# Kernel optimization log

Hardware: AMD Instinct MI355X
Metric: run time of the kernel (lower is better)

The kernel has to match this reference:

```python
import jax, jax.numpy as jnp
import numpy as np

B, T, D, S, H = 1024, 365, 5, 27, 256


def setup_inputs() -> dict:
    key = jax.random.key(0)
    ks = jax.random.split(key, 12)
    sc = 0.05
    return {
        "x_dyn": jax.random.normal(ks[0], (B, T, D), dtype=jnp.float32),
        "x_stat": jax.random.normal(ks[1], (B, S), dtype=jnp.float32),
        "W_i": jax.random.normal(ks[2], (H, S), dtype=jnp.float32) * sc,
        "b_i": jnp.zeros((H,), dtype=jnp.float32),
        "W_f": jax.random.normal(ks[3], (H, D + H), dtype=jnp.float32) * sc,
        "b_f": jnp.zeros((H,), dtype=jnp.float32),
        "W_g": jax.random.normal(ks[4], (H, D + H), dtype=jnp.float32) * sc,
        "b_g": jnp.zeros((H,), dtype=jnp.float32),
        "W_o": jax.random.normal(ks[5], (H, D + H), dtype=jnp.float32) * sc,
        "b_o": jnp.zeros((H,), dtype=jnp.float32),
        "W_head": jax.random.normal(ks[6], (1, H), dtype=jnp.float32) * sc,
        "b_head": jnp.zeros((1,), dtype=jnp.float32),
    }


def _ealstm(x_dyn, x_stat, W_i, b_i, W_f, b_f, W_g, b_g, W_o, b_o, W_head, b_head):
    d = x_dyn.shape[-1]
    # static input gate (computed once, constant over time)
    i_gate = jax.nn.sigmoid(x_stat @ W_i.T + b_i)  # [B, H]
    # split concat-weights into dyn-input and hidden parts; precompute x projections
    W_fx, W_fh = W_f[:, :d], W_f[:, d:]
    W_gx, W_gh = W_g[:, :d], W_g[:, d:]
    W_ox, W_oh = W_o[:, :d], W_o[:, d:]
    pre_f = jnp.einsum("btd,hd->tbh", x_dyn, W_fx) + b_f  # [T, B, H]
    pre_g = jnp.einsum("btd,hd->tbh", x_dyn, W_gx) + b_g
    pre_o = jnp.einsum("btd,hd->tbh", x_dyn, W_ox) + b_o

    bsz = x_dyn.shape[0]
    h0 = jnp.zeros((bsz, W_f.shape[0]), dtype=x_dyn.dtype)
    c0 = jnp.zeros_like(h0)

    def step(carry, xs):
        h, c = carry
        pf, pg, po = xs
        f = jax.nn.sigmoid(pf + h @ W_fh.T)
        g = jnp.tanh(pg + h @ W_gh.T)
        o = jax.nn.sigmoid(po + h @ W_oh.T)
        c = f * c + i_gate * g
        h = o * jnp.tanh(c)
        return (h, c), None

    (h, _), _ = jax.lax.scan(step, (h0, c0), (pre_f, pre_g, pre_o))
    # dropout is identity in eval mode
    return h @ W_head.T + b_head  # [B, 1]


def reference(x_dyn, x_stat, W_i, b_i, W_f, b_f, W_g, b_g, W_o, b_o, W_head, b_head):
    return _ealstm(x_dyn, x_stat, W_i, b_i, W_f, b_f, W_g, b_g, W_o, b_o, W_head, b_head)
```

## Files before the change

kernel.cpp:

```cpp
#include <hip/hip_runtime.h>

#define HID  256
#define DDYN 5
#define NS   27
#define TS   365
#define BS   4
#define NW   16
#define UPW  16
#define NTILE 3
#define AR   5
#define SA   272
#define G3   768

typedef short short8 __attribute__((ext_vector_type(8)));
typedef float f32x4  __attribute__((ext_vector_type(4)));

__device__ __forceinline__ unsigned short f2bf(float f) {
    union { float f; unsigned u; } v; v.f = f;
    unsigned r = v.u + 0x7FFFu + ((v.u >> 16) & 1u);
    return (unsigned short)(r >> 16);
}
__device__ __forceinline__ float bf2f(unsigned short s) {
    union { unsigned u; float f; } v; v.u = ((unsigned)s) << 16;
    return v.f;
}
__device__ __forceinline__ float bf2f_s(short s) {
    union { unsigned u; float f; } v; v.u = ((unsigned)(unsigned short)s) << 16;
    return v.f;
}
__device__ __forceinline__ float fsig(float x) {
    float e = __builtin_amdgcn_exp2f(-1.4426950408889634f * x);
    return __builtin_amdgcn_rcpf(1.0f + e);
}
__device__ __forceinline__ float ftanh(float x) {
    float e = __builtin_amdgcn_exp2f(2.8853900817779268f * x);
    return 1.0f - 2.0f * __builtin_amdgcn_rcpf(1.0f + e);
}

__global__ __launch_bounds__(1024)
void ealstm_kernel(const float* __restrict__ x_dyn,  const float* __restrict__ x_stat,
                   const float* __restrict__ W_i,    const float* __restrict__ b_i,
                   const float* __restrict__ W_f,    const float* __restrict__ b_f,
                   const float* __restrict__ W_g,    const float* __restrict__ b_g,
                   const float* __restrict__ W_o,    const float* __restrict__ b_o,
                   const float* __restrict__ W_head, const float* __restrict__ b_head,
                   float* __restrict__ out)
{
    __shared__ __align__(16) unsigned short Abuf[2][AR * SA];
    __shared__ __align__(16) float          pre[NW * 192];
    __shared__ __align__(16) unsigned short WxL[G3 * 8];
    __shared__ __align__(16) unsigned short xcA[TS * 4 * 8];
    __shared__ __align__(16) float          xst[BS * NS];
    __shared__ __align__(16) float          igL[NW * 64];

    const int tid  = threadIdx.x;
    const int bid  = blockIdx.x;
    const int b0   = bid * BS;
    const int lane = tid & 63;
    const int wv   = tid >> 6;
    const int q    = lane >> 4;
    const int n    = lane & 15;
    const int up   = lane >> 2;
    const int r    = lane & 3;
    const int u    = wv * UPW + up;

    for (int i = tid; i < 2 * AR * SA / 2; i += 1024)
        ((unsigned int*)Abuf)[i] = 0u;
    for (int i = tid; i < BS * NS; i += 1024)
        xst[i] = x_stat[(b0 + i / NS) * NS + (i % NS)];
    for (int i = tid; i < TS * BS; i += 1024) {
        int t = i >> 2, rr = i & 3;
        const float* xp = x_dyn + ((size_t)(b0 + rr) * TS + t) * DDYN;
        unsigned short* dst = &xcA[(unsigned)i * 8];
        #pragma unroll
        for (int d = 0; d < DDYN; d++) dst[d] = f2bf(xp[d]);
        dst[5] = 0x3F80; dst[6] = 0; dst[7] = 0;
    }
    if (tid < G3) {
        int col = tid;
        int gate = col >> 8, hc = col & 255;
        const float* Wg = gate == 0 ? W_f : (gate == 1 ? W_g : W_o);
        const float* bg = gate == 0 ? b_f : (gate == 1 ? b_g : b_o);
        #pragma unroll
        for (int d = 0; d < DDYN; d++) WxL[col * 8 + d] = f2bf(Wg[hc * (DDYN + HID) + d]);
        WxL[col * 8 + 5] = f2bf(bg[hc]);
        WxL[col * 8 + 6] = 0; WxL[col * 8 + 7] = 0;
    }

    short8 Bf[NTILE][8];
    #pragma unroll
    for (int j = 0; j < NTILE; j++) {
        int urow = wv * UPW + n;
        const float* Wg = j == 0 ? W_f : (j == 1 ? W_g : W_o);
        const float* wrow = Wg + urow * (DDYN + HID) + DDYN;
        #pragma unroll
        for (int c = 0; c < 8; c++) {
            int k0 = c * 32 + q * 8;
            short8 fr;
            #pragma unroll
            for (int e = 0; e < 8; e++) fr[e] = (short)f2bf(wrow[k0 + e]);
            Bf[j][c] = fr;
        }
    }
    __syncthreads();

    float cst = 0.f;
    {
        float a = b_i[u];
        for (int s = 0; s < NS; s++)
            a += xst[r * NS + s] * W_i[u * NS + s];
        igL[tid] = fsig(a);
    }
    __syncthreads();

    const int aoff  = (n < 4 ? n : 4) * SA;
    const int pbase = wv * 192 + lane;

#define STEP(PA, PB, T)                                                        \
    {                                                                          \
        f32x4 acc[NTILE];                                                      \
        _Pragma("unroll")                                                      \
        for (int j = 0; j < NTILE; j++) acc[j] = (f32x4){0.f, 0.f, 0.f, 0.f}; \
        _Pragma("unroll")                                                      \
        for (int c = 0; c < 8; c++) {                                          \
            short8 a = *(const short8*)&(PA)[aoff + c * 32 + q * 8];           \
            _Pragma("unroll")                                                  \
            for (int j = 0; j < NTILE; j++)                                    \
                acc[j] = __builtin_amdgcn_mfma_f32_16x16x32_bf16(              \
                    a, Bf[j][c], acc[j], 0, 0, 0);                             \
            __asm__ volatile("" ::: "memory");                                 \
        }                                                                      \
        if (q == 0) {                                                          \
            _Pragma("unroll")                                                  \
            for (int j = 0; j < NTILE; j++)                                    \
                *(f32x4*)&pre[wv * 192 + j * 64 + n * 4] = acc[j];             \
        }                                                                      \
        __asm__ volatile("s_waitcnt lgkmcnt(0)" ::: "memory");                 \
        {                                                                      \
            short8 xv = *(const short8*)&xcA[(unsigned)((T) * 4 + r) * 8];     \
            short8 wf = *(const short8*)&WxL[(u)        * 8];                  \
            short8 wg = *(const short8*)&WxL[(256 + u)  * 8];                  \
            short8 wo = *(const short8*)&WxL[(512 + u)  * 8];                  \
            float ig = igL[tid];                                               \
            float pf = pre[pbase]       + bf2f_s(wf[5]);                       \
            float pg = pre[pbase + 64]  + bf2f_s(wg[5]);                       \
            float po = pre[pbase + 128] + bf2f_s(wo[5]);                       \
            _Pragma("unroll")                                                  \
            for (int d = 0; d < DDYN; d++) {                                   \
                float xd = bf2f_s(xv[d]);                                      \
                pf += xd * bf2f_s(wf[d]);                                      \
                pg += xd * bf2f_s(wg[d]);                                      \
                po += xd * bf2f_s(wo[d]);                                      \
            }                                                                  \
            float f  = fsig(pf);                                               \
            float g_ = ftanh(pg);                                              \
            float o  = fsig(po);                                               \
            cst = f * cst + ig * g_;                                           \
            float h = o * ftanh(cst);                                          \
            (PB)[r * SA + u] = f2bf(h);                                        \
        }                                                                      \
        __syncthreads();                                                       \
    }

    {
        unsigned short* const A0 = &Abuf[0][0];
        unsigned short* const A1 = &Abuf[1][0];
        for (int tp = 0; tp < 182; tp++) {
            const int t0 = tp * 2;
            STEP(A0, A1, t0);
            STEP(A1, A0, t0 + 1);
        }
        STEP(A0, A1, 364);
    }
#undef STEP

    {
        float h = bf2f(Abuf[1][r * SA + u]);
        pre[u * 4 + r] = h * W_head[u];
    }
    __syncthreads();
    if (tid < 64) {
        f32x4 s = *(const f32x4*)&pre[tid * 4];
        #pragma unroll
        for (int k = 1; k < 4; k++) {
            f32x4 v = *(const f32x4*)&pre[(tid + k * 64) * 4];
            #pragma unroll
            for (int rr = 0; rr < BS; rr++) s[rr] += v[rr];
        }
        #pragma unroll
        for (int off = 32; off > 0; off >>= 1)
            #pragma unroll
            for (int rr = 0; rr < BS; rr++) s[rr] += __shfl_down(s[rr], off, 64);
        if (tid == 0) {
            float bh = b_head[0];
            #pragma unroll
            for (int rr = 0; rr < BS; rr++) out[b0 + rr] = s[rr] + bh;
        }
    }
}

extern "C" void kernel_launch(void* const* d_in, const int* in_sizes, int n_in,
                              void* d_out, int out_size, void* d_ws, size_t ws_size,
                              hipStream_t stream) {
    ealstm_kernel<<<256, 1024, 0, stream>>>(
        (const float*)d_in[0],  (const float*)d_in[1],  (const float*)d_in[2],
        (const float*)d_in[3],  (const float*)d_in[4],  (const float*)d_in[5],
        (const float*)d_in[6],  (const float*)d_in[7],  (const float*)d_in[8],
        (const float*)d_in[9],  (const float*)d_in[10], (const float*)d_in[11],
        (float*)d_out);
}
```

Before: 617.7 us.

## Halve block to 8 waves, each computing 32 hidden units per step

Shrinks the block from 1024 to 512 threads. Each wave now owns 32 hidden units using 6 MFMA tiles, and each thread updates two cell states. The static input gate stays in registers instead of shared memory. The aim is to cut barrier and wave-scheduling overhead per timestep, at the cost of a longer serial MFMA chain per wave. It also doubles the register-resident weight fragments, and with __launch_bounds__(512,2) that risks register spills.

```diff
diff --git a/kernel.cpp b/kernel.cpp
--- a/kernel.cpp
+++ b/kernel.cpp
@@ -5,9 +5,9 @@
 #define NS   27
 #define TS   365
 #define BS   4
-#define NW   16
-#define UPW  16
-#define NTILE 3
+#define NW   8
+#define UPW  32
+#define NTILE 6
 #define AR   5
 #define SA   272
 #define G3   768
@@ -37,7 +37,7 @@
     return 1.0f - 2.0f * __builtin_amdgcn_rcpf(1.0f + e);
 }
 
-__global__ __launch_bounds__(1024)
+__global__ __launch_bounds__(512, 2)
 void ealstm_kernel(const float* __restrict__ x_dyn,  const float* __restrict__ x_stat,
                    const float* __restrict__ W_i,    const float* __restrict__ b_i,
                    const float* __restrict__ W_f,    const float* __restrict__ b_f,
@@ -47,11 +47,10 @@
                    float* __restrict__ out)
 {
     __shared__ __align__(16) unsigned short Abuf[2][AR * SA];
-    __shared__ __align__(16) float          pre[NW * 192];
+    __shared__ __align__(16) float          pre[NW * 384];
     __shared__ __align__(16) unsigned short WxL[G3 * 8];
     __shared__ __align__(16) unsigned short xcA[TS * 4 * 8];
     __shared__ __align__(16) float          xst[BS * NS];
-    __shared__ __align__(16) float          igL[NW * 64];
 
     const int tid  = threadIdx.x;
     const int bid  = blockIdx.x;
@@ -62,13 +61,14 @@
     const int n    = lane & 15;
     const int up   = lane >> 2;
     const int r    = lane & 3;
-    const int u    = wv * UPW + up;
-
-    for (int i = tid; i < 2 * AR * SA / 2; i += 1024)
+    const int u_lo = wv * UPW + up;
+    const int u_hi = u_lo + 16;
+
+    for (int i = tid; i < 2 * AR * SA / 2; i += 512)
         ((unsigned int*)Abuf)[i] = 0u;
-    for (int i = tid; i < BS * NS; i += 1024)
+    for (int i = tid; i < BS * NS; i += 512)
         xst[i] = x_stat[(b0 + i / NS) * NS + (i % NS)];
-    for (int i = tid; i < TS * BS; i += 1024) {
+    for (int i = tid; i < TS * BS; i += 512) {
         int t = i >> 2, rr = i & 3;
         const float* xp = x_dyn + ((size_t)(b0 + rr) * TS + t) * DDYN;
         unsigned short* dst = &xcA[(unsigned)i * 8];
@@ -76,8 +76,7 @@
         for (int d = 0; d < DDYN; d++) dst[d] = f2bf(xp[d]);
         dst[5] = 0x3F80; dst[6] = 0; dst[7] = 0;
     }
-    if (tid < G3) {
-        int col = tid;
+    for (int col = tid; col < G3; col += 512) {
         int gate = col >> 8, hc = col & 255;
         const float* Wg = gate == 0 ? W_f : (gate == 1 ? W_g : W_o);
         const float* bg = gate == 0 ? b_f : (gate == 1 ? b_g : b_o);
@@ -90,8 +89,9 @@
     short8 Bf[NTILE][8];
     #pragma unroll
     for (int j = 0; j < NTILE; j++) {
-        int urow = wv * UPW + n;
-        const float* Wg = j == 0 ? W_f : (j == 1 ? W_g : W_o);
+        int g    = (j >= 3) ? (j - 3) : j;
+        int urow = wv * UPW + ((j >= 3) ? 16 : 0) + n;
+        const float* Wg = g == 0 ? W_f : (g == 1 ? W_g : W_o);
         const float* wrow = Wg + urow * (DDYN + HID) + DDYN;
         #pragma unroll
         for (int c = 0; c < 8; c++) {
@@ -104,17 +104,20 @@
     }
     __syncthreads();
 
-    float cst = 0.f;
+    float ig_lo, ig_hi, cst_lo = 0.f, cst_hi = 0.f;
     {
-        float a = b_i[u];
-        for (int s = 0; s < NS; s++)
-            a += xst[r * NS + s] * W_i[u * NS + s];
-        igL[tid] = fsig(a);
+        float a0 = b_i[u_lo], a1 = b_i[u_hi];
+        for (int s = 0; s < NS; s++) {
+            float xs = xst[r * NS + s];
+            a0 += xs * W_i[u_lo * NS + s];
+            a1 += xs * W_i[u_hi * NS + s];
+        }
+        ig_lo = fsig(a0); ig_hi = fsig(a1);
     }
     __syncthreads();
 
     const int aoff  = (n < 4 ? n : 4) * SA;
-    const int pbase = wv * 192 + lane;
+    const int pbase = wv * 384 + lane;
 
 #define STEP(PA, PB, T)                                                        \
     {                                                                          \
@@ -133,31 +136,55 @@
         if (q == 0) {                                                          \
             _Pragma("unroll")                                                  \
             for (int j = 0; j < NTILE; j++)                                    \
-                *(f32x4*)&pre[wv * 192 + j * 64 + n * 4] = acc[j];             \
+                *(f32x4*)&pre[wv * 384 + j * 64 + n * 4] = acc[j];             \
         }                                                                      \
         __asm__ volatile("s_waitcnt lgkmcnt(0)" ::: "memory");                 \
         {                                                                      \
             short8 xv = *(const short8*)&xcA[(unsigned)((T) * 4 + r) * 8];     \
-            short8 wf = *(const short8*)&WxL[(u)        * 8];                  \
-            short8 wg = *(const short8*)&WxL[(256 + u)  * 8];                  \
-            short8 wo = *(const short8*)&WxL[(512 + u)  * 8];                  \
-            float ig = igL[tid];                                               \
-            float pf = pre[pbase]       + bf2f_s(wf[5]);                       \
-            float pg = pre[pbase + 64]  + bf2f_s(wg[5]);                       \
-            float po = pre[pbase + 128] + bf2f_s(wo[5]);                       \
-            _Pragma("unroll")                                                  \
-            for (int d = 0; d < DDYN; d++) {                                   \
-                float xd = bf2f_s(xv[d]);                                      \
-                pf += xd * bf2f_s(wf[d]);                                      \
-                pg += xd * bf2f_s(wg[d]);                                      \
-                po += xd * bf2f_s(wo[d]);                                      \
+                                                                  \
+            {                                                                  \
+                short8 wf = *(const short8*)&WxL[(u_lo)        * 8];           \
+                short8 wg = *(const short8*)&WxL[(256 + u_lo)  * 8];           \
+                short8 wo = *(const short8*)&WxL[(512 + u_lo)  * 8];           \
+                float pf = pre[pbase]       + bf2f_s(wf[5]);                   \
+                float pg = pre[pbase + 64]  + bf2f_s(wg[5]);                   \
+                float po = pre[pbase + 128] + bf2f_s(wo[5]);                   \
+                _Pragma("unroll")                                              \
+                for (int d = 0; d < DDYN; d++) {                               \
+                    float xd = bf2f_s(xv[d]);                                  \
+                    pf += xd * bf2f_s(wf[d]);                                  \
+                    pg += xd * bf2f_s(wg[d]);                                  \
+                    po += xd * bf2f_s(wo[d]);                                  \
+                }                                                              \
+                float f  = fsig(pf);                                           \
+                float g_ = ftanh(pg);                                          \
+                float o  = fsig(po);                                           \
+                cst_lo = f * cst_lo + ig_lo * g_;                              \
+                float h = o * ftanh(cst_lo);                                   \
+                (PB)[r * SA + u_lo] = f2bf(h);                                 \
             }                                                                  \
-            float f  = fsig(pf);                                               \
-            float g_ = ftanh(pg);                                              \
-            float o  = fsig(po);                                               \
-            cst = f * cst + ig * g_;                                           \
-            float h = o * ftanh(cst);                                          \
-            (PB)[r * SA + u] = f2bf(h);                                        \
+                                                                  \
+            {                                                                  \
+                short8 wf = *(const short8*)&WxL[(u_hi)        * 8];           \
+                short8 wg = *(const short8*)&WxL[(256 + u_hi)  * 8];           \
+                short8 wo = *(const short8*)&WxL[(512 + u_hi)  * 8];           \
+                float pf = pre[pbase + 192] + bf2f_s(wf[5]);                   \
+                float pg = pre[pbase + 256] + bf2f_s(wg[5]);                   \
+                float po = pre[pbase + 320] + bf2f_s(wo[5]);                   \
+                _Pragma("unroll")                                              \
+                for (int d = 0; d < DDYN; d++) {                               \
+                    float xd = bf2f_s(xv[d]);                                  \
+                    pf += xd * bf2f_s(wf[d]);                                  \
+                    pg += xd * bf2f_s(wg[d]);                                  \
+                    po += xd * bf2f_s(wo[d]);                                  \
+                }                                                              \
+                float f  = fsig(pf);                                           \
+                float g_ = ftanh(pg);                                          \
+                float o  = fsig(po);                                           \
+                cst_hi = f * cst_hi + ig_hi * g_;                              \
+                float h = o * ftanh(cst_hi);                                   \
+                (PB)[r * SA + u_hi] = f2bf(h);                                 \
+            }                                                                  \
         }                                                                      \
         __syncthreads();                                                       \
     }
@@ -175,8 +202,10 @@
 #undef STEP
 
     {
-        float h = bf2f(Abuf[1][r * SA + u]);
-        pre[u * 4 + r] = h * W_head[u];
+        float h0 = bf2f(Abuf[1][r * SA + u_lo]);
+        pre[u_lo * 4 + r] = h0 * W_head[u_lo];
+        float h1 = bf2f(Abuf[1][r * SA + u_hi]);
+        pre[u_hi * 4 + r] = h1 * W_head[u_hi];
     }
     __syncthreads();
     if (tid < 64) {
@@ -202,7 +231,7 @@
 extern "C" void kernel_launch(void* const* d_in, const int* in_sizes, int n_in,
                               void* d_out, int out_size, void* d_ws, size_t ws_size,
                               hipStream_t stream) {
-    ealstm_kernel<<<256, 1024, 0, stream>>>(
+    ealstm_kernel<<<256, 512, 0, stream>>>(
         (const float*)d_in[0],  (const float*)d_in[1],  (const float*)d_in[2],
         (const float*)d_in[3],  (const float*)d_in[4],  (const float*)d_in[5],
         (const float*)d_in[6],  (const float*)d_in[7],  (const float*)d_in[8],
```

Result: slower. 695.5 us (+12.6%).
